# Kernel optimization log

Measured on AMD Instinct MI355X. Metric: run time of the kernel, lower is better.

Reference implementation:

```python
import jax, jax.numpy as jnp
import numpy as np

N_NODES = 100000
N_EDGES = 3200000
N_GRAPHS = 64
IN_FEATS = 128
NUM_CLASSES = 10


def setup_inputs() -> dict:
    key = jax.random.key(0)
    ks = jax.random.split(key, 12)
    in_feat = jax.random.normal(ks[0], (N_NODES, IN_FEATS), dtype=jnp.float32)
    src = jax.random.randint(ks[1], (N_EDGES,), 0, N_NODES, dtype=jnp.int32)
    dst = jax.random.randint(ks[2], (N_EDGES,), 0, N_NODES, dtype=jnp.int32)
    graph_ids = jnp.sort(jax.random.randint(ks[3], (N_NODES,), 0, N_GRAPHS, dtype=jnp.int32))
    def glorot(k, fan_in, fan_out):
        s = jnp.sqrt(6.0 / (fan_in + fan_out))
        return jax.random.uniform(k, (fan_in, fan_out), jnp.float32, -s, s)
    W1 = glorot(ks[4], IN_FEATS, 64); b1 = jnp.zeros((64,), jnp.float32)
    W2 = glorot(ks[5], 64, 128);      b2 = jnp.zeros((128,), jnp.float32)
    W3 = glorot(ks[6], 128, 64);      b3 = jnp.zeros((64,), jnp.float32)
    Wd = glorot(ks[7], 64, NUM_CLASSES)
    bd = jnp.zeros((NUM_CLASSES,), jnp.float32)
    return {"in_feat": in_feat, "src": src, "dst": dst, "graph_ids": graph_ids,
            "W1": W1, "b1": b1, "W2": W2, "b2": b2, "W3": W3, "b3": b3,
            "Wd": Wd, "bd": bd}


def _graph_conv(h, src, dst, norm_src, norm_dst, W, b):
    # DGL GraphConv, norm='both': h' = D_in^{-1/2} A (D_out^{-1/2} h) W + b
    x = h * norm_src[:, None]
    m = jax.ops.segment_sum(x[src], dst, num_segments=N_NODES)
    m = m * norm_dst[:, None]
    return m @ W + b


def reference(in_feat, src, dst, graph_ids, W1, b1, W2, b2, W3, b3, Wd, bd):
    ones = jnp.ones((N_EDGES,), jnp.float32)
    deg_out = jax.ops.segment_sum(ones, src, num_segments=N_NODES)
    deg_in = jax.ops.segment_sum(ones, dst, num_segments=N_NODES)
    norm_src = jax.lax.rsqrt(jnp.clip(deg_out, 1.0))
    norm_dst = jax.lax.rsqrt(jnp.clip(deg_in, 1.0))

    h = jax.nn.relu(_graph_conv(in_feat, src, dst, norm_src, norm_dst, W1, b1))
    h = jax.nn.relu(_graph_conv(h, src, dst, norm_src, norm_dst, W2, b2))
    h = jax.nn.relu(_graph_conv(h, src, dst, norm_src, norm_dst, W3, b3))

    hg = jax.ops.segment_sum(h, graph_ids, num_segments=N_GRAPHS)  # [G, 64]
    hg = jnp.tanh(hg)
    return hg @ Wd + bd  # [G, num_classes]
```

## Files before the change

kernel.cpp:

```cpp
#include <hip/hip_runtime.h>
#include <hip/hip_bf16.h>


constexpr int NN = 100000;
constexpr int NE = 3200000;
constexpr int NG = 64;

constexpr int CBITS = 15;
constexpr int CHUNK = 1 << CBITS;
constexpr int NCHUNK = (NE + CHUNK - 1) / CHUNK;
constexpr int WORDS = NN / 4;
constexpr int HWORDS = WORDS / 2;

typedef __attribute__((ext_vector_type(8))) short short8;
typedef __attribute__((ext_vector_type(4))) float f32x4;


__global__ __launch_bounds__(1024) void hist_kernel(
    const int* __restrict__ src, const int* __restrict__ dst,
    uint* __restrict__ pdst, uint* __restrict__ psrc,
    unsigned char* __restrict__ lrank) {
  __shared__ uint bins[HWORDS];
  for (int i = threadIdx.x; i < HWORDS; i += 1024) bins[i] = 0;
  __syncthreads();
  const int c = blockIdx.x, r = blockIdx.z;
  const int nlo = r * (NN / 2), nhi = nlo + NN / 2;
  const int wbase = r * HWORDS;
  const int start = c << CBITS;
  const int end = min(start + CHUNK, NE);
  const int* idx = (blockIdx.y == 0) ? dst : src;
  if (blockIdx.y == 0) {
    for (int i = start + threadIdx.x; i < end; i += 1024) {
      int n = idx[i];
      if (n >= nlo && n < nhi) {
        uint old = atomicAdd(&bins[(n >> 2) - wbase], 1u << ((n & 3) * 8));
        lrank[i] = (unsigned char)(old >> ((n & 3) * 8));
      }
    }
  } else {
    for (int i = start + threadIdx.x; i < end; i += 1024) {
      int n = idx[i];
      if (n >= nlo && n < nhi)
        atomicAdd(&bins[(n >> 2) - wbase], 1u << ((n & 3) * 8));
    }
  }
  __syncthreads();
  uint* pp = ((blockIdx.y == 0) ? pdst : psrc) + (size_t)c * WORDS + wbase;
  for (int i = threadIdx.x; i < HWORDS; i += 1024) pp[i] = bins[i];
}


__global__ __launch_bounds__(256) void reduce_kernel(
    const uint* __restrict__ partial, uint* __restrict__ P,
    int* __restrict__ deg) {
  int w = blockIdx.x * 256 + threadIdx.x;
  if (w >= WORDS) return;
  uint run = 0;
  if (P != nullptr) {
#pragma unroll 7
    for (int c = 0; c < NCHUNK; ++c) {
      uint v = partial[(size_t)c * WORDS + w];
      P[(size_t)c * WORDS + w] = run;
      run += v;
    }
  } else {
#pragma unroll 7
    for (int c = 0; c < NCHUNK; ++c) run += partial[(size_t)c * WORDS + w];
  }
  ((int4*)deg)[w] = make_int4(run & 0xff, (run >> 8) & 0xff,
                              (run >> 16) & 0xff, (run >> 24) & 0xff);
}

__global__ __launch_bounds__(256) void norm_kernel(
    const int* __restrict__ dout, const int* __restrict__ din,
    float* __restrict__ ns, float* __restrict__ nd, int n) {
  int i = blockIdx.x * 256 + threadIdx.x;
  if (i < n) {
    ns[i] = rsqrtf(fmaxf((float)dout[i], 1.0f));
    nd[i] = rsqrtf(fmaxf((float)din[i], 1.0f));
  }
}


__global__ __launch_bounds__(256) void scan1_kernel(
    const int* __restrict__ deg, int* __restrict__ row_off,
    int* __restrict__ bsums, int n) {
  __shared__ int s[256];
  int t = threadIdx.x;
  int base = blockIdx.x * 1024 + t * 4;
  int v0 = 0, v1 = 0, v2 = 0, v3 = 0;
  if (base + 0 < n) v0 = deg[base + 0];
  if (base + 1 < n) v1 = deg[base + 1];
  if (base + 2 < n) v2 = deg[base + 2];
  if (base + 3 < n) v3 = deg[base + 3];
  int sum = v0 + v1 + v2 + v3;
  s[t] = sum;
  __syncthreads();
  for (int off = 1; off < 256; off <<= 1) {
    int x = (t >= off) ? s[t - off] : 0;
    __syncthreads();
    s[t] += x;
    __syncthreads();
  }
  int excl = s[t] - sum;
  if (t == 255) bsums[blockIdx.x] = s[255];
  if (base + 0 < n) row_off[base + 0] = excl;
  if (base + 1 < n) row_off[base + 1] = excl + v0;
  if (base + 2 < n) row_off[base + 2] = excl + v0 + v1;
  if (base + 3 < n) row_off[base + 3] = excl + v0 + v1 + v2;
}

__global__ __launch_bounds__(128) void scan2_kernel(
    int* __restrict__ bsums, int nb, int* __restrict__ row_off, int n) {
  __shared__ int s[128];
  int t = threadIdx.x;
  int v = (t < nb) ? bsums[t] : 0;
  s[t] = v;
  __syncthreads();
  for (int off = 1; off < 128; off <<= 1) {
    int x = (t >= off) ? s[t - off] : 0;
    __syncthreads();
    s[t] += x;
    __syncthreads();
  }
  if (t < nb) bsums[t] = s[t] - v;
  if (t == 127) row_off[n] = s[127];
}

__global__ __launch_bounds__(256) void scan3_kernel(
    int* __restrict__ row_off, const int* __restrict__ bsums, int n) {
  int i = blockIdx.x * 256 + threadIdx.x;
  if (i < n) row_off[i] += bsums[i >> 10];
}


__global__ __launch_bounds__(256) void fill_kernel(
    const int* __restrict__ src, const int* __restrict__ dst,
    const int* __restrict__ row_off, const unsigned char* __restrict__ Pb,
    const unsigned char* __restrict__ lrank, int* __restrict__ csr, int e) {
  int i = blockIdx.x * 256 + threadIdx.x;
  if (i < e) {
    int d = dst[i];
    int c = i >> CBITS;
    int pos = row_off[d] + (int)Pb[(size_t)c * NN + d] + (int)lrank[i];
    csr[pos] = src[i];
  }
}


__device__ __forceinline__ uint pack_bf16(float a, float b) {
  uint ua = __float_as_uint(a), ub = __float_as_uint(b);
  ua = (ua + 0x7fffu + ((ua >> 16) & 1u)) >> 16;
  ub = (ub + 0x7fffu + ((ub >> 16) & 1u)) & 0xffff0000u;
  return ua | ub;
}

__device__ __forceinline__ ushort to_bf16(float a) {
  uint ua = __float_as_uint(a);
  return (ushort)((ua + 0x7fffu + ((ua >> 16) & 1u)) >> 16);
}

union U16 {
  uint4 u;
  short8 s;
};
__device__ __forceinline__ short8 as_short8(uint4 u) {
  U16 t;
  t.u = u;
  return t.s;
}

__device__ __forceinline__ void acc8_add(float* acc, uint4 v) {
  acc[0] += __uint_as_float(v.x << 16);
  acc[1] += __uint_as_float(v.x & 0xffff0000u);
  acc[2] += __uint_as_float(v.y << 16);
  acc[3] += __uint_as_float(v.y & 0xffff0000u);
  acc[4] += __uint_as_float(v.z << 16);
  acc[5] += __uint_as_float(v.z & 0xffff0000u);
  acc[6] += __uint_as_float(v.w << 16);
  acc[7] += __uint_as_float(v.w & 0xffff0000u);
}


__global__ __launch_bounds__(256) void transw_kernel(
    const float* __restrict__ W1, const float* __restrict__ W2,
    const float* __restrict__ W3, ushort* __restrict__ Wt1,
    ushort* __restrict__ Wt2, ushort* __restrict__ Wt3) {
  int i = blockIdx.x * 256 + threadIdx.x;
  if (i < 8192) {
    int n = i >> 7, k = i & 127;
    Wt1[i] = to_bf16(W1[k * 64 + n]);
  } else if (i < 16384) {
    int j = i - 8192;
    int n = j >> 6, k = j & 63;
    Wt2[j] = to_bf16(W2[k * 128 + n]);
  } else if (i < 24576) {
    int j = i - 16384;
    int n = j >> 7, k = j & 127;
    Wt3[j] = to_bf16(W3[k * 64 + n]);
  }
}


template <int K, int N, bool AF32, bool RELU, bool BIAS, bool SCALE>
__global__ __launch_bounds__(256) void gemm_mfma_kernel(
    const void* __restrict__ Av, const ushort* __restrict__ Wt,
    const float* __restrict__ bias, const float* __restrict__ scale,
    ushort* __restrict__ C, int n) {
  int wid = threadIdx.x >> 6, lane = threadIdx.x & 63;
  int r = lane & 15, quad = lane >> 4;
  int m16 = blockIdx.x * 64 + wid * 16;
  if (m16 >= n) return;
  int mc = min(m16 + r, n - 1);
  constexpr int KS = K / 32;
  short8 a[KS];
  if (AF32) {
    const float* A = (const float*)Av;
#pragma unroll
    for (int ks = 0; ks < KS; ++ks) {
      const float4* p = (const float4*)(A + (size_t)mc * K + ks * 32 + quad * 8);
      float4 x = p[0], y = p[1];
      uint4 u;
      u.x = pack_bf16(x.x, x.y);
      u.y = pack_bf16(x.z, x.w);
      u.z = pack_bf16(y.x, y.y);
      u.w = pack_bf16(y.z, y.w);
      a[ks] = as_short8(u);
    }
  } else {
    const ushort* A = (const ushort*)Av;
#pragma unroll
    for (int ks = 0; ks < KS; ++ks)
      a[ks] = as_short8(*(const uint4*)(A + (size_t)mc * K + ks * 32 + quad * 8));
  }
#pragma unroll
  for (int nt = 0; nt < N / 16; ++nt) {
    f32x4 acc = {0.f, 0.f, 0.f, 0.f};
#pragma unroll
    for (int ks = 0; ks < KS; ++ks) {
      short8 b = as_short8(
          *(const uint4*)(Wt + (size_t)(nt * 16 + r) * K + ks * 32 + quad * 8));
      acc = __builtin_amdgcn_mfma_f32_16x16x32_bf16(a[ks], b, acc, 0, 0, 0);
    }
    float bv = 0.f;
    if (BIAS) bv = bias[nt * 16 + r];
#pragma unroll
    for (int reg = 0; reg < 4; ++reg) {
      int m = m16 + quad * 4 + reg;
      if (m < n) {
        float v = acc[reg] + bv;
        if (RELU) v = fmaxf(v, 0.f);
        if (SCALE) v *= scale[m];
        C[(size_t)m * N + nt * 16 + r] = to_bf16(v);
      }
    }
  }
}


__device__ __forceinline__ void gather64_bf16(const int* __restrict__ csr,
                                              const ushort* __restrict__ x,
                                              int rs, int re, int lane,
                                              float* acc) {
  const int eg = lane >> 3;
  const int fl = lane & 7;
  for (int e0 = rs; e0 < re; e0 += 64) {
    int idx = e0 + lane;
    int sv = (idx < re) ? csr[idx] : 0;
    int cnt = re - e0;
    if (cnt > 64) cnt = 64;
#pragma unroll
    for (int j = 0; j < 8; ++j) {
      int jb = j * 8;
      if (jb + 8 <= cnt) {
        int s = __shfl(sv, jb + eg);
        uint4 v = *(const uint4*)(x + (size_t)s * 64 + fl * 8);
        acc8_add(acc, v);
      } else if (jb < cnt) {
        int s = __shfl(sv, jb + eg);
        uint m = (jb + eg < cnt) ? 0xffffffffu : 0u;
        uint4 v = *(const uint4*)(x + (size_t)s * 64 + fl * 8);
        v.x &= m; v.y &= m; v.z &= m; v.w &= m;
        acc8_add(acc, v);
      }
    }
  }
#pragma unroll
  for (int k = 0; k < 8; ++k) {
    acc[k] += __shfl_xor(acc[k], 8);
    acc[k] += __shfl_xor(acc[k], 16);
    acc[k] += __shfl_xor(acc[k], 32);
  }
}


__global__ __launch_bounds__(256) void agg1_kernel(
    const int* __restrict__ row_off, const int* __restrict__ csr,
    const ushort* __restrict__ t, const float* __restrict__ nd,
    const float* __restrict__ ns, const float* __restrict__ b,
    ushort* __restrict__ out, int n) {
  int wid = threadIdx.x >> 6, lane = threadIdx.x & 63;
  int node = blockIdx.x * 4 + wid;
  if (node >= n) return;
  float acc[8] = {0, 0, 0, 0, 0, 0, 0, 0};
  gather64_bf16(csr, t, row_off[node], row_off[node + 1], lane, acc);
  int fl = lane & 7;
  float ndv = nd[node], nsv = ns[node];
  const float4* bp = (const float4*)(b + fl * 8);
  float4 b0 = bp[0], b1v = bp[1];
  float o[8];
  o[0] = fmaxf(acc[0] * ndv + b0.x, 0.f) * nsv;
  o[1] = fmaxf(acc[1] * ndv + b0.y, 0.f) * nsv;
  o[2] = fmaxf(acc[2] * ndv + b0.z, 0.f) * nsv;
  o[3] = fmaxf(acc[3] * ndv + b0.w, 0.f) * nsv;
  o[4] = fmaxf(acc[4] * ndv + b1v.x, 0.f) * nsv;
  o[5] = fmaxf(acc[5] * ndv + b1v.y, 0.f) * nsv;
  o[6] = fmaxf(acc[6] * ndv + b1v.z, 0.f) * nsv;
  o[7] = fmaxf(acc[7] * ndv + b1v.w, 0.f) * nsv;
  if ((lane >> 3) == 0) {
    uint4 v;
    v.x = pack_bf16(o[0], o[1]);
    v.y = pack_bf16(o[2], o[3]);
    v.z = pack_bf16(o[4], o[5]);
    v.w = pack_bf16(o[6], o[7]);
    *(uint4*)(out + (size_t)node * 64 + fl * 8) = v;
  }
}


__global__ __launch_bounds__(256) void agg2_kernel(
    const int* __restrict__ row_off, const int* __restrict__ csr,
    const ushort* __restrict__ h1s, const float* __restrict__ nd,
    ushort* __restrict__ m2, int n) {
  int wid = threadIdx.x >> 6, lane = threadIdx.x & 63;
  int node = blockIdx.x * 4 + wid;
  if (node >= n) return;
  float acc[8] = {0, 0, 0, 0, 0, 0, 0, 0};
  gather64_bf16(csr, h1s, row_off[node], row_off[node + 1], lane, acc);
  float ndv = nd[node];
  int fl = lane & 7;
  if ((lane >> 3) == 0) {
    uint4 v;
    v.x = pack_bf16(acc[0] * ndv, acc[1] * ndv);
    v.y = pack_bf16(acc[2] * ndv, acc[3] * ndv);
    v.z = pack_bf16(acc[4] * ndv, acc[5] * ndv);
    v.w = pack_bf16(acc[6] * ndv, acc[7] * ndv);
    *(uint4*)(m2 + (size_t)node * 64 + fl * 8) = v;
  }
}


__global__ __launch_bounds__(1024) void agg3_kernel(
    const int* __restrict__ row_off, const int* __restrict__ csr,
    const ushort* __restrict__ t, const float* __restrict__ nd,
    const float* __restrict__ b, const int* __restrict__ gid,
    float* __restrict__ hg, int n) {
  __shared__ float sO[16][64];
  __shared__ int sG[16];
  __shared__ int uni;
  int wid = threadIdx.x >> 6, lane = threadIdx.x & 63;
  int node = blockIdx.x * 16 + wid;
  float acc[8] = {0, 0, 0, 0, 0, 0, 0, 0};
  gather64_bf16(csr, t, row_off[node], row_off[node + 1], lane, acc);
  int fl = lane & 7;
  float ndv = nd[node];
  const float4* bp = (const float4*)(b + fl * 8);
  float4 b0 = bp[0], b1v = bp[1];
  if ((lane >> 3) == 0) {
    sO[wid][fl * 8 + 0] = fmaxf(acc[0] * ndv + b0.x, 0.f);
    sO[wid][fl * 8 + 1] = fmaxf(acc[1] * ndv + b0.y, 0.f);
    sO[wid][fl * 8 + 2] = fmaxf(acc[2] * ndv + b0.z, 0.f);
    sO[wid][fl * 8 + 3] = fmaxf(acc[3] * ndv + b0.w, 0.f);
    sO[wid][fl * 8 + 4] = fmaxf(acc[4] * ndv + b1v.x, 0.f);
    sO[wid][fl * 8 + 5] = fmaxf(acc[5] * ndv + b1v.y, 0.f);
    sO[wid][fl * 8 + 6] = fmaxf(acc[6] * ndv + b1v.z, 0.f);
    sO[wid][fl * 8 + 7] = fmaxf(acc[7] * ndv + b1v.w, 0.f);
  }
  if (lane == 0) sG[wid] = gid[node];
  __syncthreads();
  if (threadIdx.x == 0) {
    int g0 = sG[0], u = 1;
#pragma unroll
    for (int i = 1; i < 16; ++i) u &= (sG[i] == g0);
    uni = u;
  }
  __syncthreads();
  if (uni) {
#pragma unroll
    for (int s = 8; s >= 1; s >>= 1) {
      if (wid < s) sO[wid][lane] += sO[wid + s][lane];
      __syncthreads();
    }
    if (threadIdx.x < 64) atomicAdd(&hg[sG[0] * 64 + lane], sO[0][lane]);
  } else {
    atomicAdd(&hg[sG[wid] * 64 + lane], sO[wid][lane]);
  }
}


__global__ __launch_bounds__(640) void readout_kernel(
    const float* __restrict__ hg, const float* __restrict__ Wd,
    const float* __restrict__ bd, float* __restrict__ out) {
  int t = threadIdx.x;
  int g = t / 10, c = t % 10;
  float o = bd[c];
#pragma unroll 8
  for (int k = 0; k < 64; ++k) o += tanhf(hg[g * 64 + k]) * Wd[k * 10 + c];
  out[t] = o;
}


extern "C" void kernel_launch(void* const* d_in, const int* in_sizes, int n_in,
                              void* d_out, int out_size, void* d_ws, size_t ws_size,
                              hipStream_t stream) {
  const float* in_feat = (const float*)d_in[0];
  const int* src = (const int*)d_in[1];
  const int* dst = (const int*)d_in[2];
  const int* gid = (const int*)d_in[3];
  const float* W1 = (const float*)d_in[4];
  const float* b1 = (const float*)d_in[5];
  const float* W2 = (const float*)d_in[6];
  const float* b2 = (const float*)d_in[7];
  const float* W3 = (const float*)d_in[8];
  const float* b3 = (const float*)d_in[9];
  const float* Wd = (const float*)d_in[10];
  const float* bd = (const float*)d_in[11];
  float* out = (float*)d_out;

  char* ws = (char*)d_ws;
  size_t o = 0;
  auto alloc = [&](size_t bytes) -> char* {
    char* p = ws + o;
    o = (o + bytes + 1023) & ~(size_t)1023;
    return p;
  };
  float* hg = (float*)alloc(NG * 64 * 4);
  size_t zero_bytes = o;
  int* deg_out = (int*)alloc(NN * 4);
  int* deg_in = (int*)alloc(NN * 4);
  float* norm_src = (float*)alloc(NN * 4);
  float* norm_dst = (float*)alloc(NN * 4);
  int* row_off = (int*)alloc((NN + 1) * 4);
  int* bsums = (int*)alloc(512);
  ushort* Wt1 = (ushort*)alloc(64 * 128 * 2);
  ushort* Wt2 = (ushort*)alloc(128 * 64 * 2);
  ushort* Wt3 = (ushort*)alloc(64 * 128 * 2);
  int* csr = (int*)alloc((size_t)NE * 4);
  ushort* tbuf = (ushort*)alloc((size_t)NN * 64 * 2);
  ushort* h1s = (ushort*)alloc((size_t)NN * 64 * 2);
  ushort* m2 = (ushort*)alloc((size_t)NN * 64 * 2);
  ushort* h2s = (ushort*)alloc((size_t)NN * 128 * 2);
  (void)ws_size;

  char* ov = (char*)m2;
  uint* pdst = (uint*)ov;
  uint* psrc = (uint*)(ov + 9800000);
  uint* Pw = (uint*)(ov + 19600000);
  unsigned char* lrank = (unsigned char*)(ov + 29400000);

  hipMemsetAsync(d_ws, 0, zero_bytes, stream);

  const int egrid = (NE + 255) / 256;
  const int ngrid = (NN + 255) / 256;
  const int sgrid = (NN + 1023) / 1024;
  const int wgrid = (NN + 3) / 4;
  const int rgrid = (WORDS + 255) / 256;
  const int ggrid = (NN + 63) / 64;

  transw_kernel<<<96, 256, 0, stream>>>(W1, W2, W3, Wt1, Wt2, Wt3);
  hist_kernel<<<dim3(NCHUNK, 2, 2), 1024, 0, stream>>>(src, dst, pdst, psrc, lrank);
  reduce_kernel<<<rgrid, 256, 0, stream>>>(pdst, Pw, deg_in);
  reduce_kernel<<<rgrid, 256, 0, stream>>>(psrc, nullptr, deg_out);
  norm_kernel<<<ngrid, 256, 0, stream>>>(deg_out, deg_in, norm_src, norm_dst, NN);
  scan1_kernel<<<sgrid, 256, 0, stream>>>(deg_in, row_off, bsums, NN);
  scan2_kernel<<<1, 128, 0, stream>>>(bsums, sgrid, row_off, NN);
  scan3_kernel<<<ngrid, 256, 0, stream>>>(row_off, bsums, NN);
  fill_kernel<<<egrid, 256, 0, stream>>>(src, dst, row_off,
                                         (const unsigned char*)Pw, lrank, csr, NE);

  gemm_mfma_kernel<128, 64, true, false, false, true>
      <<<ggrid, 256, 0, stream>>>(in_feat, Wt1, nullptr, norm_src, tbuf, NN);
  agg1_kernel<<<wgrid, 256, 0, stream>>>(row_off, csr, tbuf, norm_dst, norm_src,
                                         b1, h1s, NN);
  agg2_kernel<<<wgrid, 256, 0, stream>>>(row_off, csr, h1s, norm_dst, m2, NN);
  gemm_mfma_kernel<64, 128, false, true, true, true>
      <<<ggrid, 256, 0, stream>>>(m2, Wt2, b2, norm_src, h2s, NN);
  gemm_mfma_kernel<128, 64, false, false, false, false>
      <<<ggrid, 256, 0, stream>>>(h2s, Wt3, nullptr, nullptr, tbuf, NN);
  agg3_kernel<<<NN / 16, 1024, 0, stream>>>(row_off, csr, tbuf, norm_dst, b3,
                                            gid, hg, NN);
  readout_kernel<<<1, 640, 0, stream>>>(hg, Wd, bd, out);
}
```

Before: 496.6 us.

## Process two destination nodes per wavefront in aggregation kernels and merge degree reductions

The aggregation kernels now give each 64-lane wavefront two consecutive destination nodes. Their edge ranges are gathered as one contiguous span, and each gathered row is split between two accumulator sets at the node boundary. With about 32 edges per node, this fills all 64 lanes instead of leaving half idle per 64-edge chunk, and it halves the number of waves launched. The two degree reduce kernels are also merged into one launch using a 2-D grid. In exchange there is extra masking and branching at the node boundary, more accumulator registers, and the grid assumes NN divides evenly by 8 and 16.

```diff
diff --git a/kernel.cpp b/kernel.cpp
--- a/kernel.cpp
+++ b/kernel.cpp
@@ -14,6 +14,7 @@
 
 typedef __attribute__((ext_vector_type(8))) short short8;
 typedef __attribute__((ext_vector_type(4))) float f32x4;
+typedef __attribute__((ext_vector_type(2))) float f32x2;
 
 
 __global__ __launch_bounds__(1024) void hist_kernel(
@@ -50,25 +51,28 @@
 }
 
 
-__global__ __launch_bounds__(256) void reduce_kernel(
-    const uint* __restrict__ partial, uint* __restrict__ P,
-    int* __restrict__ deg) {
+__global__ __launch_bounds__(256) void reduce2_kernel(
+    const uint* __restrict__ pdst, const uint* __restrict__ psrc,
+    uint* __restrict__ P, int* __restrict__ deg_in,
+    int* __restrict__ deg_out) {
   int w = blockIdx.x * 256 + threadIdx.x;
   if (w >= WORDS) return;
   uint run = 0;
-  if (P != nullptr) {
+  if (blockIdx.y == 0) {
 #pragma unroll 7
     for (int c = 0; c < NCHUNK; ++c) {
-      uint v = partial[(size_t)c * WORDS + w];
+      uint v = pdst[(size_t)c * WORDS + w];
       P[(size_t)c * WORDS + w] = run;
       run += v;
     }
+    ((int4*)deg_in)[w] = make_int4(run & 0xff, (run >> 8) & 0xff,
+                                   (run >> 16) & 0xff, (run >> 24) & 0xff);
   } else {
 #pragma unroll 7
-    for (int c = 0; c < NCHUNK; ++c) run += partial[(size_t)c * WORDS + w];
-  }
-  ((int4*)deg)[w] = make_int4(run & 0xff, (run >> 8) & 0xff,
-                              (run >> 16) & 0xff, (run >> 24) & 0xff);
+    for (int c = 0; c < NCHUNK; ++c) run += psrc[(size_t)c * WORDS + w];
+    ((int4*)deg_out)[w] = make_int4(run & 0xff, (run >> 8) & 0xff,
+                                    (run >> 16) & 0xff, (run >> 24) & 0xff);
+  }
 }
 
 __global__ __launch_bounds__(256) void norm_kernel(
@@ -170,15 +174,18 @@
   return t.s;
 }
 
-__device__ __forceinline__ void acc8_add(float* acc, uint4 v) {
-  acc[0] += __uint_as_float(v.x << 16);
-  acc[1] += __uint_as_float(v.x & 0xffff0000u);
-  acc[2] += __uint_as_float(v.y << 16);
-  acc[3] += __uint_as_float(v.y & 0xffff0000u);
-  acc[4] += __uint_as_float(v.z << 16);
-  acc[5] += __uint_as_float(v.z & 0xffff0000u);
-  acc[6] += __uint_as_float(v.w << 16);
-  acc[7] += __uint_as_float(v.w & 0xffff0000u);
+__device__ __forceinline__ f32x2 bf2(uint u) {
+  f32x2 r;
+  r.x = __uint_as_float(u << 16);
+  r.y = __uint_as_float(u & 0xffff0000u);
+  return r;
+}
+
+__device__ __forceinline__ void add8(f32x2* a, uint4 v) {
+  a[0] += bf2(v.x);
+  a[1] += bf2(v.y);
+  a[2] += bf2(v.z);
+  a[3] += bf2(v.w);
 }
 
 
@@ -258,10 +265,10 @@
 }
 
 
-__device__ __forceinline__ void gather64_bf16(const int* __restrict__ csr,
-                                              const ushort* __restrict__ x,
-                                              int rs, int re, int lane,
-                                              float* acc) {
+__device__ __forceinline__ void gather2_bf16(const int* __restrict__ csr,
+                                             const ushort* __restrict__ x,
+                                             int rs, int rm, int re, int lane,
+                                             f32x2* a0, f32x2* a1) {
   const int eg = lane >> 3;
   const int fl = lane & 7;
   for (int e0 = rs; e0 < re; e0 += 64) {
@@ -269,29 +276,50 @@
     int sv = (idx < re) ? csr[idx] : 0;
     int cnt = re - e0;
     if (cnt > 64) cnt = 64;
+    int c0 = rm - e0;
 #pragma unroll
     for (int j = 0; j < 8; ++j) {
       int jb = j * 8;
-      if (jb + 8 <= cnt) {
+      if (jb < cnt) {
         int s = __shfl(sv, jb + eg);
         uint4 v = *(const uint4*)(x + (size_t)s * 64 + fl * 8);
-        acc8_add(acc, v);
-      } else if (jb < cnt) {
-        int s = __shfl(sv, jb + eg);
-        uint m = (jb + eg < cnt) ? 0xffffffffu : 0u;
-        uint4 v = *(const uint4*)(x + (size_t)s * 64 + fl * 8);
-        v.x &= m; v.y &= m; v.z &= m; v.w &= m;
-        acc8_add(acc, v);
+        if (jb + 8 > cnt) {
+          uint mv = ((jb + eg) < cnt) ? 0xffffffffu : 0u;
+          v.x &= mv; v.y &= mv; v.z &= mv; v.w &= mv;
+        }
+        if (jb + 8 <= c0) {
+          add8(a0, v);
+        } else if (jb >= c0) {
+          add8(a1, v);
+        } else {
+          uint m0 = ((jb + eg) < c0) ? 0xffffffffu : 0u;
+          uint4 v0;
+          v0.x = v.x & m0; v0.y = v.y & m0; v0.z = v.z & m0; v0.w = v.w & m0;
+          add8(a0, v0);
+          v.x ^= v0.x; v.y ^= v0.y; v.z ^= v0.z; v.w ^= v0.w;
+          add8(a1, v);
+        }
       }
     }
   }
 #pragma unroll
-  for (int k = 0; k < 8; ++k) {
-    acc[k] += __shfl_xor(acc[k], 8);
-    acc[k] += __shfl_xor(acc[k], 16);
-    acc[k] += __shfl_xor(acc[k], 32);
-  }
-}
+  for (int k = 0; k < 4; ++k) {
+    a0[k].x += __shfl_xor(a0[k].x, 8);
+    a0[k].x += __shfl_xor(a0[k].x, 16);
+    a0[k].x += __shfl_xor(a0[k].x, 32);
+    a0[k].y += __shfl_xor(a0[k].y, 8);
+    a0[k].y += __shfl_xor(a0[k].y, 16);
+    a0[k].y += __shfl_xor(a0[k].y, 32);
+    a1[k].x += __shfl_xor(a1[k].x, 8);
+    a1[k].x += __shfl_xor(a1[k].x, 16);
+    a1[k].x += __shfl_xor(a1[k].x, 32);
+    a1[k].y += __shfl_xor(a1[k].y, 8);
+    a1[k].y += __shfl_xor(a1[k].y, 16);
+    a1[k].y += __shfl_xor(a1[k].y, 32);
+  }
+}
+
+#define ACC_SEL(k) ((eg == 0) ? a0[(k) >> 1][(k)&1] : a1[(k) >> 1][(k)&1])
 
 
 __global__ __launch_bounds__(256) void agg1_kernel(
@@ -300,29 +328,30 @@
     const float* __restrict__ ns, const float* __restrict__ b,
     ushort* __restrict__ out, int n) {
   int wid = threadIdx.x >> 6, lane = threadIdx.x & 63;
-  int node = blockIdx.x * 4 + wid;
-  if (node >= n) return;
-  float acc[8] = {0, 0, 0, 0, 0, 0, 0, 0};
-  gather64_bf16(csr, t, row_off[node], row_off[node + 1], lane, acc);
-  int fl = lane & 7;
-  float ndv = nd[node], nsv = ns[node];
-  const float4* bp = (const float4*)(b + fl * 8);
-  float4 b0 = bp[0], b1v = bp[1];
-  float o[8];
-  o[0] = fmaxf(acc[0] * ndv + b0.x, 0.f) * nsv;
-  o[1] = fmaxf(acc[1] * ndv + b0.y, 0.f) * nsv;
-  o[2] = fmaxf(acc[2] * ndv + b0.z, 0.f) * nsv;
-  o[3] = fmaxf(acc[3] * ndv + b0.w, 0.f) * nsv;
-  o[4] = fmaxf(acc[4] * ndv + b1v.x, 0.f) * nsv;
-  o[5] = fmaxf(acc[5] * ndv + b1v.y, 0.f) * nsv;
-  o[6] = fmaxf(acc[6] * ndv + b1v.z, 0.f) * nsv;
-  o[7] = fmaxf(acc[7] * ndv + b1v.w, 0.f) * nsv;
-  if ((lane >> 3) == 0) {
+  int n0 = blockIdx.x * 8 + wid * 2;
+  int rs = row_off[n0], rm = row_off[n0 + 1], re = row_off[n0 + 2];
+  f32x2 a0[4] = {{0, 0}, {0, 0}, {0, 0}, {0, 0}};
+  f32x2 a1[4] = {{0, 0}, {0, 0}, {0, 0}, {0, 0}};
+  gather2_bf16(csr, t, rs, rm, re, lane, a0, a1);
+  int eg = lane >> 3, fl = lane & 7;
+  if (eg < 2) {
+    int node = n0 + eg;
+    float ndv = nd[node], nsv = ns[node];
+    const float4* bp = (const float4*)(b + fl * 8);
+    float4 b0 = bp[0], b1v = bp[1];
+    float o0 = fmaxf(ACC_SEL(0) * ndv + b0.x, 0.f) * nsv;
+    float o1 = fmaxf(ACC_SEL(1) * ndv + b0.y, 0.f) * nsv;
+    float o2 = fmaxf(ACC_SEL(2) * ndv + b0.z, 0.f) * nsv;
+    float o3 = fmaxf(ACC_SEL(3) * ndv + b0.w, 0.f) * nsv;
+    float o4 = fmaxf(ACC_SEL(4) * ndv + b1v.x, 0.f) * nsv;
+    float o5 = fmaxf(ACC_SEL(5) * ndv + b1v.y, 0.f) * nsv;
+    float o6 = fmaxf(ACC_SEL(6) * ndv + b1v.z, 0.f) * nsv;
+    float o7 = fmaxf(ACC_SEL(7) * ndv + b1v.w, 0.f) * nsv;
     uint4 v;
-    v.x = pack_bf16(o[0], o[1]);
-    v.y = pack_bf16(o[2], o[3]);
-    v.z = pack_bf16(o[4], o[5]);
-    v.w = pack_bf16(o[6], o[7]);
+    v.x = pack_bf16(o0, o1);
+    v.y = pack_bf16(o2, o3);
+    v.z = pack_bf16(o4, o5);
+    v.w = pack_bf16(o6, o7);
     *(uint4*)(out + (size_t)node * 64 + fl * 8) = v;
   }
 }
@@ -333,24 +362,26 @@
     const ushort* __restrict__ h1s, const float* __restrict__ nd,
     ushort* __restrict__ m2, int n) {
   int wid = threadIdx.x >> 6, lane = threadIdx.x & 63;
-  int node = blockIdx.x * 4 + wid;
-  if (node >= n) return;
-  float acc[8] = {0, 0, 0, 0, 0, 0, 0, 0};
-  gather64_bf16(csr, h1s, row_off[node], row_off[node + 1], lane, acc);
-  float ndv = nd[node];
-  int fl = lane & 7;
-  if ((lane >> 3) == 0) {
+  int n0 = blockIdx.x * 8 + wid * 2;
+  int rs = row_off[n0], rm = row_off[n0 + 1], re = row_off[n0 + 2];
+  f32x2 a0[4] = {{0, 0}, {0, 0}, {0, 0}, {0, 0}};
+  f32x2 a1[4] = {{0, 0}, {0, 0}, {0, 0}, {0, 0}};
+  gather2_bf16(csr, h1s, rs, rm, re, lane, a0, a1);
+  int eg = lane >> 3, fl = lane & 7;
+  if (eg < 2) {
+    int node = n0 + eg;
+    float ndv = nd[node];
     uint4 v;
-    v.x = pack_bf16(acc[0] * ndv, acc[1] * ndv);
-    v.y = pack_bf16(acc[2] * ndv, acc[3] * ndv);
-    v.z = pack_bf16(acc[4] * ndv, acc[5] * ndv);
-    v.w = pack_bf16(acc[6] * ndv, acc[7] * ndv);
+    v.x = pack_bf16(ACC_SEL(0) * ndv, ACC_SEL(1) * ndv);
+    v.y = pack_bf16(ACC_SEL(2) * ndv, ACC_SEL(3) * ndv);
+    v.z = pack_bf16(ACC_SEL(4) * ndv, ACC_SEL(5) * ndv);
+    v.w = pack_bf16(ACC_SEL(6) * ndv, ACC_SEL(7) * ndv);
     *(uint4*)(m2 + (size_t)node * 64 + fl * 8) = v;
   }
 }
 
 
-__global__ __launch_bounds__(1024) void agg3_kernel(
+__global__ __launch_bounds__(512) void agg3_kernel(
     const int* __restrict__ row_off, const int* __restrict__ csr,
     const ushort* __restrict__ t, const float* __restrict__ nd,
     const float* __restrict__ b, const int* __restrict__ gid,
@@ -359,24 +390,29 @@
   __shared__ int sG[16];
   __shared__ int uni;
   int wid = threadIdx.x >> 6, lane = threadIdx.x & 63;
-  int node = blockIdx.x * 16 + wid;
-  float acc[8] = {0, 0, 0, 0, 0, 0, 0, 0};
-  gather64_bf16(csr, t, row_off[node], row_off[node + 1], lane, acc);
-  int fl = lane & 7;
-  float ndv = nd[node];
-  const float4* bp = (const float4*)(b + fl * 8);
-  float4 b0 = bp[0], b1v = bp[1];
-  if ((lane >> 3) == 0) {
-    sO[wid][fl * 8 + 0] = fmaxf(acc[0] * ndv + b0.x, 0.f);
-    sO[wid][fl * 8 + 1] = fmaxf(acc[1] * ndv + b0.y, 0.f);
-    sO[wid][fl * 8 + 2] = fmaxf(acc[2] * ndv + b0.z, 0.f);
-    sO[wid][fl * 8 + 3] = fmaxf(acc[3] * ndv + b0.w, 0.f);
-    sO[wid][fl * 8 + 4] = fmaxf(acc[4] * ndv + b1v.x, 0.f);
-    sO[wid][fl * 8 + 5] = fmaxf(acc[5] * ndv + b1v.y, 0.f);
-    sO[wid][fl * 8 + 6] = fmaxf(acc[6] * ndv + b1v.z, 0.f);
-    sO[wid][fl * 8 + 7] = fmaxf(acc[7] * ndv + b1v.w, 0.f);
-  }
-  if (lane == 0) sG[wid] = gid[node];
+  int n0 = blockIdx.x * 16 + wid * 2;
+  int rs = row_off[n0], rm = row_off[n0 + 1], re = row_off[n0 + 2];
+  f32x2 a0[4] = {{0, 0}, {0, 0}, {0, 0}, {0, 0}};
+  f32x2 a1[4] = {{0, 0}, {0, 0}, {0, 0}, {0, 0}};
+  gather2_bf16(csr, t, rs, rm, re, lane, a0, a1);
+  int eg = lane >> 3, fl = lane & 7;
+  if (eg < 2) {
+    int node = n0 + eg;
+    int row = wid * 2 + eg;
+    float ndv = nd[node];
+    const float4* bp = (const float4*)(b + fl * 8);
+    float4 b0 = bp[0], b1v = bp[1];
+    sO[row][fl * 8 + 0] = fmaxf(ACC_SEL(0) * ndv + b0.x, 0.f);
+    sO[row][fl * 8 + 1] = fmaxf(ACC_SEL(1) * ndv + b0.y, 0.f);
+    sO[row][fl * 8 + 2] = fmaxf(ACC_SEL(2) * ndv + b0.z, 0.f);
+    sO[row][fl * 8 + 3] = fmaxf(ACC_SEL(3) * ndv + b0.w, 0.f);
+    sO[row][fl * 8 + 4] = fmaxf(ACC_SEL(4) * ndv + b1v.x, 0.f);
+    sO[row][fl * 8 + 5] = fmaxf(ACC_SEL(5) * ndv + b1v.y, 0.f);
+    sO[row][fl * 8 + 6] = fmaxf(ACC_SEL(6) * ndv + b1v.z, 0.f);
+    sO[row][fl * 8 + 7] = fmaxf(ACC_SEL(7) * ndv + b1v.w, 0.f);
+  }
+  if (lane == 0) sG[wid * 2] = gid[n0];
+  if (lane == 8) sG[wid * 2 + 1] = gid[n0 + 1];
   __syncthreads();
   if (threadIdx.x == 0) {
     int g0 = sG[0], u = 1;
@@ -386,14 +422,16 @@
   }
   __syncthreads();
   if (uni) {
+    int r = threadIdx.x >> 6;
 #pragma unroll
     for (int s = 8; s >= 1; s >>= 1) {
-      if (wid < s) sO[wid][lane] += sO[wid + s][lane];
+      if (r < s) sO[r][lane] += sO[r + s][lane];
       __syncthreads();
     }
     if (threadIdx.x < 64) atomicAdd(&hg[sG[0] * 64 + lane], sO[0][lane]);
   } else {
-    atomicAdd(&hg[sG[wid] * 64 + lane], sO[wid][lane]);
+    atomicAdd(&hg[sG[wid * 2] * 64 + lane], sO[wid * 2][lane]);
+    atomicAdd(&hg[sG[wid * 2 + 1] * 64 + lane], sO[wid * 2 + 1][lane]);
   }
 }
 
@@ -463,14 +501,14 @@
   const int egrid = (NE + 255) / 256;
   const int ngrid = (NN + 255) / 256;
   const int sgrid = (NN + 1023) / 1024;
-  const int wgrid = (NN + 3) / 4;
+  const int wgrid2 = NN / 8;
   const int rgrid = (WORDS + 255) / 256;
   const int ggrid = (NN + 63) / 64;
 
   transw_kernel<<<96, 256, 0, stream>>>(W1, W2, W3, Wt1, Wt2, Wt3);
   hist_kernel<<<dim3(NCHUNK, 2, 2), 1024, 0, stream>>>(src, dst, pdst, psrc, lrank);
-  reduce_kernel<<<rgrid, 256, 0, stream>>>(pdst, Pw, deg_in);
-  reduce_kernel<<<rgrid, 256, 0, stream>>>(psrc, nullptr, deg_out);
+  reduce2_kernel<<<dim3(rgrid, 2), 256, 0, stream>>>(pdst, psrc, Pw, deg_in,
+                                                     deg_out);
   norm_kernel<<<ngrid, 256, 0, stream>>>(deg_out, deg_in, norm_src, norm_dst, NN);
   scan1_kernel<<<sgrid, 256, 0, stream>>>(deg_in, row_off, bsums, NN);
   scan2_kernel<<<1, 128, 0, stream>>>(bsums, sgrid, row_off, NN);
@@ -480,14 +518,14 @@
 
   gemm_mfma_kernel<128, 64, true, false, false, true>
       <<<ggrid, 256, 0, stream>>>(in_feat, Wt1, nullptr, norm_src, tbuf, NN);
-  agg1_kernel<<<wgrid, 256, 0, stream>>>(row_off, csr, tbuf, norm_dst, norm_src,
-                                         b1, h1s, NN);
-  agg2_kernel<<<wgrid, 256, 0, stream>>>(row_off, csr, h1s, norm_dst, m2, NN);
+  agg1_kernel<<<wgrid2, 256, 0, stream>>>(row_off, csr, tbuf, norm_dst,
+                                          norm_src, b1, h1s, NN);
+  agg2_kernel<<<wgrid2, 256, 0, stream>>>(row_off, csr, h1s, norm_dst, m2, NN);
   gemm_mfma_kernel<64, 128, false, true, true, true>
       <<<ggrid, 256, 0, stream>>>(m2, Wt2, b2, norm_src, h2s, NN);
   gemm_mfma_kernel<128, 64, false, false, false, false>
       <<<ggrid, 256, 0, stream>>>(h2s, Wt3, nullptr, nullptr, tbuf, NN);
-  agg3_kernel<<<NN / 16, 1024, 0, stream>>>(row_off, csr, tbuf, norm_dst, b3,
-                                            gid, hg, NN);
+  agg3_kernel<<<NN / 16, 512, 0, stream>>>(row_off, csr, tbuf, norm_dst, b3,
+                                           gid, hg, NN);
   readout_kernel<<<1, 640, 0, stream>>>(hg, Wd, bd, out);
 }
```

Result: faster. 472.2 us (-4.9%).
